# Kernel tuning notes

Measured on AMD Instinct MI355X. Metric: run time of the kernel, lower is better.

The kernel has to match this reference:

```python
import jax, jax.numpy as jnp
import numpy as np
from math import sqrt

DIM = 64
N_HEADS = 12
B, T = 4, 2048


def setup_inputs() -> dict:
    key = jax.random.key(0)
    ks = jax.random.split(key, 5)
    scale = 1.0 / sqrt(DIM)
    x = jax.random.normal(ks[0], (B, T, DIM), dtype=jnp.float32)
    # torch Linear(dim, h*dim) weight is (h*dim, dim); store transposed (dim, h*dim)
    Wq = jax.random.uniform(ks[1], (DIM, N_HEADS * DIM), dtype=jnp.float32, minval=-scale, maxval=scale)
    Wk = jax.random.uniform(ks[2], (DIM, N_HEADS * DIM), dtype=jnp.float32, minval=-scale, maxval=scale)
    Wv = jax.random.uniform(ks[3], (DIM, N_HEADS * DIM), dtype=jnp.float32, minval=-scale, maxval=scale)
    # finalDense: Linear(h*dim, dim) -> stored (h*dim, dim)
    Wo = jax.random.uniform(ks[4], (N_HEADS * DIM, DIM), dtype=jnp.float32,
                            minval=-1.0 / sqrt(N_HEADS * DIM), maxval=1.0 / sqrt(N_HEADS * DIM))
    return {"x": x, "Wq": Wq, "Wk": Wk, "Wv": Wv, "Wo": Wo}


def reference(x, Wq, Wk, Wv, Wo):
    b, t, k = x.shape
    h = Wq.shape[1] // k
    # NOTE: the original module does .view(b,t,h,k).view(b*h,t,k), a flat
    # row-major memory reinterpretation (NOT a head transpose). jnp.reshape
    # is the same flat reshape, so this is faithful.
    Q = (x @ Wq).reshape(b * h, t, k)
    K = (x @ Wk).reshape(b * h, t, k)
    V = (x @ Wv).reshape(b * h, t, k)
    # W[b,i,j] = sum_k K[b,i,k] * Q[b,j,k], scaled; softmax over j (last dim)
    W = jnp.einsum('bik,bjk->bij', K, Q) / sqrt(k)
    W = jax.nn.softmax(W, axis=2)
    Z = jnp.einsum('bij,bjk->bik', W, V)  # (b*h, t, k)
    Z = Z.reshape(b, t, h * k)  # flat reinterpretation, matches torch views
    return Z @ Wo
```

## Files before the change

### kernel.cpp

```cpp
#include <hip/hip_runtime.h>
#include <hip/hip_bf16.h>


#define DIM 64
#define NH 12
#define HD 768
#define BT 8192
#define TSEQ 2048
#define NSLICE 48
#define SLICE (TSEQ*DIM)

#define LDQ 72
#define LDT 72
#define LDP 72

typedef unsigned short ushort;
typedef __attribute__((ext_vector_type(8))) short bf16x8;
typedef __attribute__((ext_vector_type(4))) short bf16x4;
typedef __attribute__((ext_vector_type(4))) float f32x4;
typedef __attribute__((ext_vector_type(16))) float f32x16;
typedef __attribute__((ext_vector_type(4))) unsigned int uint32x4;

#define SCALE2 0.18033688011112042f

__device__ __forceinline__ ushort f2b(float f) {
    union { float f; unsigned int i; } v; v.f = f;
    unsigned int x = v.i;
    return (ushort)((x + 0x7fffu + ((x >> 16) & 1u)) >> 16);
}

__global__ __launch_bounds__(256) void prep_w(
    const float* __restrict__ Wq, const float* __restrict__ Wk,
    const float* __restrict__ Wv, const float* __restrict__ Wo,
    ushort* __restrict__ Wt, ushort* __restrict__ Wot)
{
    __shared__ float tile[64][65];
    int bx = blockIdx.x;
    int z = bx / 12, bt = bx % 12;
    const float* __restrict__ IN = (z == 0) ? Wq : (z == 1) ? Wk : (z == 2) ? Wv : Wo;
    int inStride  = (z < 3) ? HD : DIM;
    int outStride = (z < 3) ? DIM : HD;
    int rbase = (z < 3) ? 0 : bt * 64;
    int cbase = (z < 3) ? bt * 64 : 0;
    ushort* __restrict__ OUT = (z < 3) ? (Wt + (size_t)z * HD * DIM) : Wot;
    int t = threadIdx.x;
    int r = t >> 2, c0 = (t & 3) * 16;
    #pragma unroll
    for (int cc = 0; cc < 16; cc += 4) {
        float4 a = *(const float4*)&IN[(size_t)(rbase + r) * inStride + cbase + c0 + cc];
        tile[r][c0 + cc] = a.x; tile[r][c0 + cc + 1] = a.y;
        tile[r][c0 + cc + 2] = a.z; tile[r][c0 + cc + 3] = a.w;
    }
    __syncthreads();
    int cl = t >> 2, r0 = (t & 3) * 16;
    ushort tmp[16] __attribute__((aligned(16)));
    #pragma unroll
    for (int rr = 0; rr < 16; ++rr) tmp[rr] = f2b(tile[r0 + rr][cl]);
    *(float4*)&OUT[(size_t)(cbase + cl) * outStride + rbase + r0] = *(const float4*)tmp;
    *(float4*)&OUT[(size_t)(cbase + cl) * outStride + rbase + r0 + 8] = *(const float4*)&tmp[8];
}

__global__ __launch_bounds__(256) void qkv_kernel(
    const float* __restrict__ x, const ushort* __restrict__ Wt,
    ushort* __restrict__ Q, ushort* __restrict__ K, ushort* __restrict__ V)
{
    int rt = blockIdx.x, yg = blockIdx.y;
    int t = threadIdx.x, w = t >> 6, lane = t & 63;
    int ln = lane & 15, q = lane >> 4;
    int m0 = rt * 64 + w * 16;

    float4 xa = *(const float4*)&x[(size_t)(m0 + ln) * DIM + q * 8];
    float4 xb_ = *(const float4*)&x[(size_t)(m0 + ln) * DIM + q * 8 + 4];
    float4 xc = *(const float4*)&x[(size_t)(m0 + ln) * DIM + 32 + q * 8];
    float4 xd = *(const float4*)&x[(size_t)(m0 + ln) * DIM + 32 + q * 8 + 4];
    ushort ta[8] __attribute__((aligned(16)));
    ushort tb[8] __attribute__((aligned(16)));
    ta[0]=f2b(xa.x); ta[1]=f2b(xa.y); ta[2]=f2b(xa.z); ta[3]=f2b(xa.w);
    ta[4]=f2b(xb_.x); ta[5]=f2b(xb_.y); ta[6]=f2b(xb_.z); ta[7]=f2b(xb_.w);
    tb[0]=f2b(xc.x); tb[1]=f2b(xc.y); tb[2]=f2b(xc.z); tb[3]=f2b(xc.w);
    tb[4]=f2b(xd.x); tb[5]=f2b(xd.y); tb[6]=f2b(xd.z); tb[7]=f2b(xd.w);
    bf16x8 af0 = *(const bf16x8*)ta;
    bf16x8 af1 = *(const bf16x8*)tb;

    for (int cc = 0; cc < 6; ++cc) {
        int ct = yg * 6 + cc;
        int which = ct / 12;
        int col0 = (ct % 12) * 64;
        const ushort* __restrict__ Wz = Wt + (size_t)which * HD * DIM;
        ushort* __restrict__ Y = (which == 0) ? Q : (which == 1) ? K : V;
        float sc = (which == 0) ? SCALE2 : 1.f;
        #pragma unroll
        for (int nt = 0; nt < 4; ++nt) {
            int n = col0 + nt * 16 + ln;
            bf16x8 bf0 = *(const bf16x8*)&Wz[(size_t)n * DIM + q * 8];
            bf16x8 bf1 = *(const bf16x8*)&Wz[(size_t)n * DIM + 32 + q * 8];
            f32x4 acc = (f32x4){0.f, 0.f, 0.f, 0.f};
            acc = __builtin_amdgcn_mfma_f32_16x16x32_bf16(af0, bf0, acc, 0, 0, 0);
            acc = __builtin_amdgcn_mfma_f32_16x16x32_bf16(af1, bf1, acc, 0, 0, 0);
            #pragma unroll
            for (int r = 0; r < 4; ++r)
                Y[(size_t)(m0 + q * 4 + r) * HD + col0 + nt * 16 + ln] = f2b(acc[r] * sc);
        }
    }
}

__global__ __launch_bounds__(256) void vtrans_kernel(
    const ushort* __restrict__ V, ushort* __restrict__ Vt)
{
    __shared__ ushort tileT[64 * LDT];
    int tt = blockIdx.x, s = blockIdx.y;
    const ushort* __restrict__ Vp = V + (size_t)s * SLICE;
    ushort* __restrict__ Vo = Vt + (size_t)s * SLICE;
    int t = threadIdx.x;
    int r = t >> 3, c = (t & 7) * 8;
    ushort va[8] __attribute__((aligned(16)));
    ushort vb[8] __attribute__((aligned(16)));
    *(float4*)va = *(const float4*)&Vp[(size_t)(tt * 64 + r) * DIM + c];
    *(float4*)vb = *(const float4*)&Vp[(size_t)(tt * 64 + r + 32) * DIM + c];
    int g0 = ((r >> 3) ^ (c >> 3)) * 8 + (r & 7);
    int g1 = (((r + 32) >> 3) ^ (c >> 3)) * 8 + (r & 7);
    #pragma unroll
    for (int k = 0; k < 8; ++k) {
        tileT[(c + k) * LDT + g0] = va[k];
        tileT[(c + k) * LDT + g1] = vb[k];
    }
    __syncthreads();
    #pragma unroll
    for (int j = 0; j < 2; ++j) {
        int flat = t + 256 * j;
        int d = flat >> 3, tg = flat & 7;
        int sg = tg ^ ((d >> 3) & 7);
        float4 vv = *(const float4*)&tileT[d * LDT + sg * 8];
        *(float4*)&Vo[(size_t)d * TSEQ + tt * 64 + tg * 8] = vv;
    }
}

__global__ __launch_bounds__(256, 3) void attn_kernel(
    const ushort* __restrict__ Qs, const ushort* __restrict__ Ks,
    const ushort* __restrict__ Vts, ushort* __restrict__ Zs)
{
    __shared__ ushort sh[4 * 64 * LDQ];
    int itile = blockIdx.x, s = blockIdx.y;
    const ushort* __restrict__ Qp = Qs + (size_t)s * SLICE;
    const ushort* __restrict__ Kp = Ks + (size_t)s * SLICE;
    const ushort* __restrict__ Vp = Vts + (size_t)s * SLICE;
    ushort* __restrict__ Zp = Zs + (size_t)s * SLICE;
    int t = threadIdx.x, w = t >> 6, lane = t & 63;
    int i5 = lane & 31, hi = lane >> 5;

    bf16x8 kf[4];
    {
        size_t krow = (size_t)(itile * 128 + w * 32 + i5) * DIM;
        #pragma unroll
        for (int c = 0; c < 4; ++c)
            kf[c] = *(const bf16x8*)&Kp[krow + c * 16 + hi * 8];
    }

    f32x16 Of0, Of1;
    #pragma unroll
    for (int r = 0; r < 16; ++r) { Of0[r] = 0.f; Of1[r] = 0.f; }
    float lsum = 0.f;

    int sr = t >> 3, sc = (t & 7) * 8;
    const ushort* qsrc0 = &Qp[(size_t)sr * DIM + sc];
    const ushort* qsrc1 = &Qp[(size_t)(sr + 32) * DIM + sc];
    const ushort* vsrc0 = &Vp[(size_t)sr * TSEQ + sc];
    const ushort* vsrc1 = &Vp[(size_t)(sr + 32) * TSEQ + sc];

    float4 qa0 = *(const float4*)qsrc0;
    float4 qa1 = *(const float4*)qsrc1;
    float4 va0 = *(const float4*)vsrc0;
    float4 va1 = *(const float4*)vsrc1;
    *(float4*)&sh[sr * LDQ + sc] = qa0;
    *(float4*)&sh[(sr + 32) * LDQ + sc] = qa1;
    *(float4*)&sh[2 * 64 * LDQ + sr * LDQ + sc] = va0;
    *(float4*)&sh[2 * 64 * LDQ + (sr + 32) * LDQ + sc] = va1;
    qa0 = *(const float4*)(qsrc0 + 64 * DIM);
    qa1 = *(const float4*)(qsrc1 + 64 * DIM);
    va0 = *(const float4*)(vsrc0 + 64);
    va1 = *(const float4*)(vsrc1 + 64);
    __syncthreads();

    for (int tt = 0; tt < 32; ++tt) {
        int ib = tt & 1;
        const ushort* Qc = sh + ib * (64 * LDQ);
        const ushort* Vc = sh + (2 + ib) * (64 * LDQ);
        if (tt < 31) {
            ushort* Qn = sh + (ib ^ 1) * (64 * LDQ);
            ushort* Vn = sh + (2 + (ib ^ 1)) * (64 * LDQ);
            *(float4*)&Qn[sr * LDQ + sc] = qa0;
            *(float4*)&Qn[(sr + 32) * LDQ + sc] = qa1;
            *(float4*)&Vn[sr * LDQ + sc] = va0;
            *(float4*)&Vn[(sr + 32) * LDQ + sc] = va1;
            if (tt < 30) {
                size_t qo = (size_t)(tt + 2) * 64 * DIM;
                int vo = (tt + 2) * 64;
                qa0 = *(const float4*)(qsrc0 + qo);
                qa1 = *(const float4*)(qsrc1 + qo);
                va0 = *(const float4*)(vsrc0 + vo);
                va1 = *(const float4*)(vsrc1 + vo);
            }
        }
        #pragma unroll
        for (int js = 0; js < 2; ++js) {
            f32x16 acc;
            #pragma unroll
            for (int r = 0; r < 16; ++r) acc[r] = 0.f;
            #pragma unroll
            for (int c = 0; c < 4; ++c) {
                bf16x8 aQ = *(const bf16x8*)&Qc[(js * 32 + i5) * LDQ + c * 16 + hi * 8];
                acc = __builtin_amdgcn_mfma_f32_32x32x16_bf16(aQ, kf[c], acc, 0, 0, 0);
            }
            unsigned wv[8];
            float ls = 0.f;
            #pragma unroll
            for (int k = 0; k < 8; ++k) {
                float p0 = __builtin_amdgcn_exp2f(acc[2 * k]);
                float p1 = __builtin_amdgcn_exp2f(acc[2 * k + 1]);
                unsigned int b0 = __float_as_uint(p0), b1 = __float_as_uint(p1);
                unsigned int t1 = b1 & 0xFFFF0000u;
                unsigned int h = (b0 >> 16) | t1;
                ls += __uint_as_float(h << 16) + __uint_as_float(t1);
                wv[k] = h;
            }
            lsum += ls;
            uint32x4 u0 = { wv[0], wv[1], wv[2], wv[3] };
            uint32x4 u1 = { wv[4], wv[5], wv[6], wv[7] };
            bf16x8 pa0 = __builtin_bit_cast(bf16x8, u0);
            bf16x8 pa1 = __builtin_bit_cast(bf16x8, u1);
            #pragma unroll
            for (int dt = 0; dt < 2; ++dt) {
                int vbase = (dt * 32 + i5) * LDQ + js * 32 + 4 * hi;
                bf16x4 v0a = *(const bf16x4*)&Vc[vbase];
                bf16x4 v0b = *(const bf16x4*)&Vc[vbase + 8];
                bf16x4 v1a = *(const bf16x4*)&Vc[vbase + 16];
                bf16x4 v1b = *(const bf16x4*)&Vc[vbase + 24];
                bf16x8 vb0 = __builtin_shufflevector(v0a, v0b, 0, 1, 2, 3, 4, 5, 6, 7);
                bf16x8 vb1 = __builtin_shufflevector(v1a, v1b, 0, 1, 2, 3, 4, 5, 6, 7);
                if (dt == 0) {
                    Of0 = __builtin_amdgcn_mfma_f32_32x32x16_bf16(pa0, vb0, Of0, 0, 0, 0);
                    Of0 = __builtin_amdgcn_mfma_f32_32x32x16_bf16(pa1, vb1, Of0, 0, 0, 0);
                } else {
                    Of1 = __builtin_amdgcn_mfma_f32_32x32x16_bf16(pa0, vb0, Of1, 0, 0, 0);
                    Of1 = __builtin_amdgcn_mfma_f32_32x32x16_bf16(pa1, vb1, Of1, 0, 0, 0);
                }
            }
        }
        __syncthreads();
    }

    float l = lsum + __shfl_xor(lsum, 32);
    float linv = 1.f / l;
    #pragma unroll
    for (int r = 0; r < 16; ++r) {
        int cr = (r & 3) + 8 * (r >> 2);
        float li = __shfl(linv, cr + 4 * hi);
        int row = w * 32 + cr + 4 * hi;
        sh[row * LDQ + i5]      = f2b(Of0[r] * li);
        sh[row * LDQ + 32 + i5] = f2b(Of1[r] * li);
    }
    __syncthreads();
    int zr = t >> 1, zc = (t & 1) * 32;
    size_t zoff = (size_t)(itile * 128 + zr) * DIM + zc;
    #pragma unroll
    for (int c4 = 0; c4 < 4; ++c4)
        *(float4*)&Zp[zoff + c4 * 8] = *(const float4*)&sh[zr * LDQ + zc + c4 * 8];
}

__global__ __launch_bounds__(64) void out_kernel(
    const ushort* __restrict__ Z, const ushort* __restrict__ Wot,
    float* __restrict__ out)
{
    int m0 = blockIdx.x * 32;
    int lane = threadIdx.x;
    int ln = lane & 15, q = lane >> 4;
    f32x4 acc[2][4];
    #pragma unroll
    for (int u = 0; u < 2; ++u)
        #pragma unroll
        for (int nt = 0; nt < 4; ++nt) acc[u][nt] = (f32x4){0.f, 0.f, 0.f, 0.f};
    for (int kc = 0; kc < 24; ++kc) {
        bf16x8 a0 = *(const bf16x8*)&Z[(size_t)(m0 + ln) * HD + kc * 32 + q * 8];
        bf16x8 a1 = *(const bf16x8*)&Z[(size_t)(m0 + 16 + ln) * HD + kc * 32 + q * 8];
        #pragma unroll
        for (int nt = 0; nt < 4; ++nt) {
            bf16x8 bf = *(const bf16x8*)&Wot[(size_t)(nt * 16 + ln) * HD + kc * 32 + q * 8];
            acc[0][nt] = __builtin_amdgcn_mfma_f32_16x16x32_bf16(a0, bf, acc[0][nt], 0, 0, 0);
            acc[1][nt] = __builtin_amdgcn_mfma_f32_16x16x32_bf16(a1, bf, acc[1][nt], 0, 0, 0);
        }
    }
    #pragma unroll
    for (int u = 0; u < 2; ++u)
        #pragma unroll
        for (int nt = 0; nt < 4; ++nt)
            #pragma unroll
            for (int r = 0; r < 4; ++r)
                out[(size_t)(m0 + u * 16 + q * 4 + r) * DIM + nt * 16 + ln] = acc[u][nt][r];
}

extern "C" void kernel_launch(void* const* d_in, const int* in_sizes, int n_in,
                              void* d_out, int out_size, void* d_ws, size_t ws_size,
                              hipStream_t stream)
{
    const float* x  = (const float*)d_in[0];
    const float* Wq = (const float*)d_in[1];
    const float* Wk = (const float*)d_in[2];
    const float* Wv = (const float*)d_in[3];
    const float* Wo = (const float*)d_in[4];
    float* out = (float*)d_out;

    const size_t n = (size_t)BT * HD;
    ushort* Q   = (ushort*)d_ws;
    ushort* K   = Q + n;
    ushort* V   = K + n;
    ushort* Vt  = V + n;
    ushort* Wt  = Vt;
    ushort* Wot = Vt + n;
    ushort* Z   = V;

    prep_w<<<48, 256, 0, stream>>>(Wq, Wk, Wv, Wo, Wt, Wot);
    qkv_kernel<<<dim3(128, 6), 256, 0, stream>>>(x, Wt, Q, K, V);
    vtrans_kernel<<<dim3(32, 48), 256, 0, stream>>>(V, Vt);
    attn_kernel<<<dim3(16, 48), 256, 0, stream>>>(Q, K, Vt, Z);
    out_kernel<<<256, 64, 0, stream>>>(Z, Wot, out);
}
```

Measured before the change: 173.5 us.

## Compute softmax denominator via MFMA and retune qkv/out kernel grids

The attention kernel stops summing bf16-rounded probabilities with scalar adds. It now accumulates the row sums with an extra MFMA against a ones vector, which also removes the cross-lane shuffles needed at normalisation. Separately, the QKV projection grid is doubled with half the column tiles per block, and the output projection uses 256-thread blocks with one 16-row tile per wave. The extra MFMAs add matrix-core work per tile in exchange for less VALU work, while the grid changes trade per-block reuse for more parallelism.

Result: slower. 179.7 us (+3.6%).

```diff
diff --git a/kernel.cpp b/kernel.cpp
--- a/kernel.cpp
+++ b/kernel.cpp
@@ -12,7 +12,6 @@
 
 #define LDQ 72
 #define LDT 72
-#define LDP 72
 
 typedef unsigned short ushort;
 typedef __attribute__((ext_vector_type(8))) short bf16x8;
@@ -82,8 +81,8 @@
     bf16x8 af0 = *(const bf16x8*)ta;
     bf16x8 af1 = *(const bf16x8*)tb;
 
-    for (int cc = 0; cc < 6; ++cc) {
-        int ct = yg * 6 + cc;
+    for (int cc = 0; cc < 3; ++cc) {
+        int ct = yg * 3 + cc;
         int which = ct / 12;
         int col0 = (ct % 12) * 64;
         const ushort* __restrict__ Wz = Wt + (size_t)which * HD * DIM;
@@ -155,11 +154,12 @@
         for (int c = 0; c < 4; ++c)
             kf[c] = *(const bf16x8*)&Kp[krow + c * 16 + hi * 8];
     }
-
-    f32x16 Of0, Of1;
-    #pragma unroll
-    for (int r = 0; r < 16; ++r) { Of0[r] = 0.f; Of1[r] = 0.f; }
-    float lsum = 0.f;
+    const uint32x4 uones = { 0x3F803F80u, 0x3F803F80u, 0x3F803F80u, 0x3F803F80u };
+    const bf16x8 ones = __builtin_bit_cast(bf16x8, uones);
+
+    f32x16 Of0, Of1, Lf;
+    #pragma unroll
+    for (int r = 0; r < 16; ++r) { Of0[r] = 0.f; Of1[r] = 0.f; Lf[r] = 0.f; }
 
     int sr = t >> 3, sc = (t & 7) * 8;
     const ushort* qsrc0 = &Qp[(size_t)sr * DIM + sc];
@@ -212,22 +212,18 @@
                 acc = __builtin_amdgcn_mfma_f32_32x32x16_bf16(aQ, kf[c], acc, 0, 0, 0);
             }
             unsigned wv[8];
-            float ls = 0.f;
             #pragma unroll
             for (int k = 0; k < 8; ++k) {
                 float p0 = __builtin_amdgcn_exp2f(acc[2 * k]);
                 float p1 = __builtin_amdgcn_exp2f(acc[2 * k + 1]);
-                unsigned int b0 = __float_as_uint(p0), b1 = __float_as_uint(p1);
-                unsigned int t1 = b1 & 0xFFFF0000u;
-                unsigned int h = (b0 >> 16) | t1;
-                ls += __uint_as_float(h << 16) + __uint_as_float(t1);
-                wv[k] = h;
+                wv[k] = (__float_as_uint(p0) >> 16) | (__float_as_uint(p1) & 0xFFFF0000u);
             }
-            lsum += ls;
             uint32x4 u0 = { wv[0], wv[1], wv[2], wv[3] };
             uint32x4 u1 = { wv[4], wv[5], wv[6], wv[7] };
             bf16x8 pa0 = __builtin_bit_cast(bf16x8, u0);
             bf16x8 pa1 = __builtin_bit_cast(bf16x8, u1);
+            Lf = __builtin_amdgcn_mfma_f32_32x32x16_bf16(pa0, ones, Lf, 0, 0, 0);
+            Lf = __builtin_amdgcn_mfma_f32_32x32x16_bf16(pa1, ones, Lf, 0, 0, 0);
             #pragma unroll
             for (int dt = 0; dt < 2; ++dt) {
                 int vbase = (dt * 32 + i5) * LDQ + js * 32 + 4 * hi;
@@ -249,12 +245,10 @@
         __syncthreads();
     }
 
-    float l = lsum + __shfl_xor(lsum, 32);
-    float linv = 1.f / l;
     #pragma unroll
     for (int r = 0; r < 16; ++r) {
         int cr = (r & 3) + 8 * (r >> 2);
-        float li = __shfl(linv, cr + 4 * hi);
+        float li = 1.f / Lf[r];
         int row = w * 32 + cr + 4 * hi;
         sh[row * LDQ + i5]      = f2b(Of0[r] * li);
         sh[row * LDQ + 32 + i5] = f2b(Of1[r] * li);
@@ -267,35 +261,29 @@
         *(float4*)&Zp[zoff + c4 * 8] = *(const float4*)&sh[zr * LDQ + zc + c4 * 8];
 }
 
-__global__ __launch_bounds__(64) void out_kernel(
+__global__ __launch_bounds__(256) void out_kernel(
     const ushort* __restrict__ Z, const ushort* __restrict__ Wot,
     float* __restrict__ out)
 {
-    int m0 = blockIdx.x * 32;
-    int lane = threadIdx.x;
+    int t = threadIdx.x, w = t >> 6, lane = t & 63;
+    int m0 = blockIdx.x * 64 + w * 16;
     int ln = lane & 15, q = lane >> 4;
-    f32x4 acc[2][4];
-    #pragma unroll
-    for (int u = 0; u < 2; ++u)
-        #pragma unroll
-        for (int nt = 0; nt < 4; ++nt) acc[u][nt] = (f32x4){0.f, 0.f, 0.f, 0.f};
+    f32x4 acc[4];
+    #pragma unroll
+    for (int nt = 0; nt < 4; ++nt) acc[nt] = (f32x4){0.f, 0.f, 0.f, 0.f};
     for (int kc = 0; kc < 24; ++kc) {
-        bf16x8 a0 = *(const bf16x8*)&Z[(size_t)(m0 + ln) * HD + kc * 32 + q * 8];
-        bf16x8 a1 = *(const bf16x8*)&Z[(size_t)(m0 + 16 + ln) * HD + kc * 32 + q * 8];
+        bf16x8 a = *(const bf16x8*)&Z[(size_t)(m0 + ln) * HD + kc * 32 + q * 8];
         #pragma unroll
         for (int nt = 0; nt < 4; ++nt) {
             bf16x8 bf = *(const bf16x8*)&Wot[(size_t)(nt * 16 + ln) * HD + kc * 32 + q * 8];
-            acc[0][nt] = __builtin_amdgcn_mfma_f32_16x16x32_bf16(a0, bf, acc[0][nt], 0, 0, 0);
-            acc[1][nt] = __builtin_amdgcn_mfma_f32_16x16x32_bf16(a1, bf, acc[1][nt], 0, 0, 0);
+            acc[nt] = __builtin_amdgcn_mfma_f32_16x16x32_bf16(a, bf, acc[nt], 0, 0, 0);
         }
     }
     #pragma unroll
-    for (int u = 0; u < 2; ++u)
-        #pragma unroll
-        for (int nt = 0; nt < 4; ++nt)
-            #pragma unroll
-            for (int r = 0; r < 4; ++r)
-                out[(size_t)(m0 + u * 16 + q * 4 + r) * DIM + nt * 16 + ln] = acc[u][nt][r];
+    for (int nt = 0; nt < 4; ++nt)
+        #pragma unroll
+        for (int r = 0; r < 4; ++r)
+            out[(size_t)(m0 + q * 4 + r) * DIM + nt * 16 + ln] = acc[nt][r];
 }
 
 extern "C" void kernel_launch(void* const* d_in, const int* in_sizes, int n_in,
@@ -319,8 +307,8 @@
     ushort* Z   = V;
 
     prep_w<<<48, 256, 0, stream>>>(Wq, Wk, Wv, Wo, Wt, Wot);
-    qkv_kernel<<<dim3(128, 6), 256, 0, stream>>>(x, Wt, Q, K, V);
+    qkv_kernel<<<dim3(128, 12), 256, 0, stream>>>(x, Wt, Q, K, V);
     vtrans_kernel<<<dim3(32, 48), 256, 0, stream>>>(V, Vt);
     attn_kernel<<<dim3(16, 48), 256, 0, stream>>>(Q, K, Vt, Z);
-    out_kernel<<<256, 64, 0, stream>>>(Z, Wot, out);
-}
+    out_kernel<<<128, 256, 0, stream>>>(Z, Wot, out);
+}
```

## Split MFMA accumulator chains, stage QKV stores via LDS, remap attention blocks per XCD

Applied to the files above, without the earlier changes.

The attention kernel splits each chain of dependent MFMAs (the QK score accumulation and the PV output accumulation) into two independent accumulators that are summed at the end. This shortens the accumulator dependency chains so consecutive MFMAs can issue back to back, at the cost of more accumulator registers. The grid index is remapped so each XCD processes a contiguous group of six slices, which should improve L2 reuse of K/V. The QKV projection now stages its output tile through shared memory so global stores are 16-byte coalesced instead of scattered 2-byte writes, which adds two block barriers per column tile.

Result: no change. 176.3 us (+1.6%).

```diff
diff --git a/kernel.cpp b/kernel.cpp
--- a/kernel.cpp
+++ b/kernel.cpp
@@ -12,7 +12,6 @@
 
 #define LDQ 72
 #define LDT 72
-#define LDP 72
 
 typedef unsigned short ushort;
 typedef __attribute__((ext_vector_type(8))) short bf16x8;
@@ -64,10 +63,12 @@
     const float* __restrict__ x, const ushort* __restrict__ Wt,
     ushort* __restrict__ Q, ushort* __restrict__ K, ushort* __restrict__ V)
 {
+    __shared__ ushort Sst[4][16 * LDT];
     int rt = blockIdx.x, yg = blockIdx.y;
     int t = threadIdx.x, w = t >> 6, lane = t & 63;
     int ln = lane & 15, q = lane >> 4;
     int m0 = rt * 64 + w * 16;
+    ushort* Sw = Sst[w];
 
     float4 xa = *(const float4*)&x[(size_t)(m0 + ln) * DIM + q * 8];
     float4 xb_ = *(const float4*)&x[(size_t)(m0 + ln) * DIM + q * 8 + 4];
@@ -82,6 +83,7 @@
     bf16x8 af0 = *(const bf16x8*)ta;
     bf16x8 af1 = *(const bf16x8*)tb;
 
+    int rr8 = lane >> 3, c8 = (lane & 7) * 8;
     for (int cc = 0; cc < 6; ++cc) {
         int ct = yg * 6 + cc;
         int which = ct / 12;
@@ -89,18 +91,30 @@
         const ushort* __restrict__ Wz = Wt + (size_t)which * HD * DIM;
         ushort* __restrict__ Y = (which == 0) ? Q : (which == 1) ? K : V;
         float sc = (which == 0) ? SCALE2 : 1.f;
+        f32x4 acc[4];
         #pragma unroll
         for (int nt = 0; nt < 4; ++nt) {
             int n = col0 + nt * 16 + ln;
             bf16x8 bf0 = *(const bf16x8*)&Wz[(size_t)n * DIM + q * 8];
             bf16x8 bf1 = *(const bf16x8*)&Wz[(size_t)n * DIM + 32 + q * 8];
-            f32x4 acc = (f32x4){0.f, 0.f, 0.f, 0.f};
-            acc = __builtin_amdgcn_mfma_f32_16x16x32_bf16(af0, bf0, acc, 0, 0, 0);
-            acc = __builtin_amdgcn_mfma_f32_16x16x32_bf16(af1, bf1, acc, 0, 0, 0);
+            f32x4 a = (f32x4){0.f, 0.f, 0.f, 0.f};
+            a = __builtin_amdgcn_mfma_f32_16x16x32_bf16(af0, bf0, a, 0, 0, 0);
+            a = __builtin_amdgcn_mfma_f32_16x16x32_bf16(af1, bf1, a, 0, 0, 0);
+            acc[nt] = a;
+        }
+        #pragma unroll
+        for (int nt = 0; nt < 4; ++nt)
             #pragma unroll
             for (int r = 0; r < 4; ++r)
-                Y[(size_t)(m0 + q * 4 + r) * HD + col0 + nt * 16 + ln] = f2b(acc[r] * sc);
-        }
+                Sw[(q * 4 + r) * LDT + nt * 16 + ln] = f2b(acc[nt][r] * sc);
+        __syncthreads();
+        #pragma unroll
+        for (int p = 0; p < 2; ++p) {
+            int rr = p * 8 + rr8;
+            float4 v = *(const float4*)&Sw[rr * LDT + c8];
+            *(float4*)&Y[(size_t)(m0 + rr) * HD + col0 + c8] = v;
+        }
+        __syncthreads();
     }
 }
 
@@ -140,7 +154,10 @@
     const ushort* __restrict__ Vts, ushort* __restrict__ Zs)
 {
     __shared__ ushort sh[4 * 64 * LDQ];
-    int itile = blockIdx.x, s = blockIdx.y;
+    int bid = blockIdx.x + (blockIdx.y << 4);
+    int xcd = bid & 7, idx = bid >> 3;
+    int s = xcd * 6 + idx % 6;
+    int itile = idx / 6;
     const ushort* __restrict__ Qp = Qs + (size_t)s * SLICE;
     const ushort* __restrict__ Kp = Ks + (size_t)s * SLICE;
     const ushort* __restrict__ Vp = Vts + (size_t)s * SLICE;
@@ -156,9 +173,9 @@
             kf[c] = *(const bf16x8*)&Kp[krow + c * 16 + hi * 8];
     }
 
-    f32x16 Of0, Of1;
-    #pragma unroll
-    for (int r = 0; r < 16; ++r) { Of0[r] = 0.f; Of1[r] = 0.f; }
+    f32x16 Of0a, Of0b, Of1a, Of1b;
+    #pragma unroll
+    for (int r = 0; r < 16; ++r) { Of0a[r] = 0.f; Of0b[r] = 0.f; Of1a[r] = 0.f; Of1b[r] = 0.f; }
     float lsum = 0.f;
 
     int sr = t >> 3, sc = (t & 7) * 8;
@@ -203,20 +220,23 @@
         }
         #pragma unroll
         for (int js = 0; js < 2; ++js) {
-            f32x16 acc;
-            #pragma unroll
-            for (int r = 0; r < 16; ++r) acc[r] = 0.f;
-            #pragma unroll
-            for (int c = 0; c < 4; ++c) {
-                bf16x8 aQ = *(const bf16x8*)&Qc[(js * 32 + i5) * LDQ + c * 16 + hi * 8];
-                acc = __builtin_amdgcn_mfma_f32_32x32x16_bf16(aQ, kf[c], acc, 0, 0, 0);
-            }
+            f32x16 sa, sb;
+            #pragma unroll
+            for (int r = 0; r < 16; ++r) { sa[r] = 0.f; sb[r] = 0.f; }
+            bf16x8 a0 = *(const bf16x8*)&Qc[(js * 32 + i5) * LDQ + 0 * 16 + hi * 8];
+            bf16x8 a1 = *(const bf16x8*)&Qc[(js * 32 + i5) * LDQ + 1 * 16 + hi * 8];
+            bf16x8 a2 = *(const bf16x8*)&Qc[(js * 32 + i5) * LDQ + 2 * 16 + hi * 8];
+            bf16x8 a3 = *(const bf16x8*)&Qc[(js * 32 + i5) * LDQ + 3 * 16 + hi * 8];
+            sa = __builtin_amdgcn_mfma_f32_32x32x16_bf16(a0, kf[0], sa, 0, 0, 0);
+            sb = __builtin_amdgcn_mfma_f32_32x32x16_bf16(a2, kf[2], sb, 0, 0, 0);
+            sa = __builtin_amdgcn_mfma_f32_32x32x16_bf16(a1, kf[1], sa, 0, 0, 0);
+            sb = __builtin_amdgcn_mfma_f32_32x32x16_bf16(a3, kf[3], sb, 0, 0, 0);
             unsigned wv[8];
             float ls = 0.f;
             #pragma unroll
             for (int k = 0; k < 8; ++k) {
-                float p0 = __builtin_amdgcn_exp2f(acc[2 * k]);
-                float p1 = __builtin_amdgcn_exp2f(acc[2 * k + 1]);
+                float p0 = __builtin_amdgcn_exp2f(sa[2 * k] + sb[2 * k]);
+                float p1 = __builtin_amdgcn_exp2f(sa[2 * k + 1] + sb[2 * k + 1]);
                 unsigned int b0 = __float_as_uint(p0), b1 = __float_as_uint(p1);
                 unsigned int t1 = b1 & 0xFFFF0000u;
                 unsigned int h = (b0 >> 16) | t1;
@@ -238,11 +258,11 @@
                 bf16x8 vb0 = __builtin_shufflevector(v0a, v0b, 0, 1, 2, 3, 4, 5, 6, 7);
                 bf16x8 vb1 = __builtin_shufflevector(v1a, v1b, 0, 1, 2, 3, 4, 5, 6, 7);
                 if (dt == 0) {
-                    Of0 = __builtin_amdgcn_mfma_f32_32x32x16_bf16(pa0, vb0, Of0, 0, 0, 0);
-                    Of0 = __builtin_amdgcn_mfma_f32_32x32x16_bf16(pa1, vb1, Of0, 0, 0, 0);
+                    Of0a = __builtin_amdgcn_mfma_f32_32x32x16_bf16(pa0, vb0, Of0a, 0, 0, 0);
+                    Of0b = __builtin_amdgcn_mfma_f32_32x32x16_bf16(pa1, vb1, Of0b, 0, 0, 0);
                 } else {
-                    Of1 = __builtin_amdgcn_mfma_f32_32x32x16_bf16(pa0, vb0, Of1, 0, 0, 0);
-                    Of1 = __builtin_amdgcn_mfma_f32_32x32x16_bf16(pa1, vb1, Of1, 0, 0, 0);
+                    Of1a = __builtin_amdgcn_mfma_f32_32x32x16_bf16(pa0, vb0, Of1a, 0, 0, 0);
+                    Of1b = __builtin_amdgcn_mfma_f32_32x32x16_bf16(pa1, vb1, Of1b, 0, 0, 0);
                 }
             }
         }
@@ -256,8 +276,8 @@
         int cr = (r & 3) + 8 * (r >> 2);
         float li = __shfl(linv, cr + 4 * hi);
         int row = w * 32 + cr + 4 * hi;
-        sh[row * LDQ + i5]      = f2b(Of0[r] * li);
-        sh[row * LDQ + 32 + i5] = f2b(Of1[r] * li);
+        sh[row * LDQ + i5]      = f2b((Of0a[r] + Of0b[r]) * li);
+        sh[row * LDQ + 32 + i5] = f2b((Of1a[r] + Of1b[r]) * li);
     }
     __syncthreads();
     int zr = t >> 1, zc = (t & 1) * 32;
```
